# Performance work log

Hardware: AMD Instinct MI355X
Metric: run time of the kernel (lower is better)

## Reference

```python
import jax, jax.numpy as jnp
import numpy as np

B, T, D = 8, 1024, 1024
F = 4 * D  # RWKV channel-mixing hidden size
EPS = 1e-3  # keras LayerNormalization default epsilon


def layer_norm(x, g, b):
    mu = jnp.mean(x, axis=-1, keepdims=True)
    var = jnp.var(x, axis=-1, keepdims=True)
    return (x - mu) * jax.lax.rsqrt(var + EPS) * g + b


def setup_inputs() -> dict:
    key = jax.random.key(0)
    ks = jax.random.split(key, 16)
    s = 0.02
    f32 = jnp.float32
    return {
        "x": jax.random.normal(ks[0], (B, T, D), f32),
        "att_x": jnp.zeros((B, D), f32),
        "att_a": jnp.zeros((B, D), f32),
        "att_b": jnp.zeros((B, D), f32),
        "att_p": jnp.zeros((B, D), f32),
        "ffn_x": jnp.zeros((B, D), f32),
        "ln1_g": jnp.ones((D,), f32),
        "ln1_b": jnp.zeros((D,), f32),
        "ln2_g": jnp.ones((D,), f32),
        "ln2_b": jnp.zeros((D,), f32),
        "tm_mix_k": jax.random.uniform(ks[1], (D,), f32),
        "tm_mix_v": jax.random.uniform(ks[2], (D,), f32),
        "tm_mix_r": jax.random.uniform(ks[3], (D,), f32),
        "tm_decay": jax.random.normal(ks[4], (D,), f32) * 0.1,
        "tm_first": jax.random.normal(ks[5], (D,), f32) * 0.1,
        "Wk": jax.random.normal(ks[6], (D, D), f32) * s,
        "Wv": jax.random.normal(ks[7], (D, D), f32) * s,
        "Wr": jax.random.normal(ks[8], (D, D), f32) * s,
        "Wo": jax.random.normal(ks[9], (D, D), f32) * s,
        "cm_mix_k": jax.random.uniform(ks[10], (D,), f32),
        "cm_mix_r": jax.random.uniform(ks[11], (D,), f32),
        "Ck": jax.random.normal(ks[12], (D, F), f32) * s,
        "Cr": jax.random.normal(ks[13], (D, D), f32) * s,
        "Cv": jax.random.normal(ks[14], (F, D), f32) * s,
    }


def _wkv_scan(k, v, aa, bb, pp, decay, first):
    # k, v: [B, T, D]; states: [B, D]. Numerically-stable RWKV-4 WKV recurrence.
    w = -jnp.exp(decay)  # per-channel decay, always negative

    def step(carry, kv):
        aa, bb, pp = carry
        k_t, v_t = kv
        ww = first + k_t
        p = jnp.maximum(pp, ww)
        e1 = jnp.exp(pp - p)
        e2 = jnp.exp(ww - p)
        wkv = (e1 * aa + e2 * v_t) / (e1 * bb + e2)
        ww2 = pp + w
        p2 = jnp.maximum(ww2, k_t)
        e1b = jnp.exp(ww2 - p2)
        e2b = jnp.exp(k_t - p2)
        return (e1b * aa + e2b * v_t, e1b * bb + e2b, p2), wkv

    kT = jnp.swapaxes(k, 0, 1)  # [T, B, D]
    vT = jnp.swapaxes(v, 0, 1)
    (aa, bb, pp), wkv = jax.lax.scan(step, (aa, bb, pp), (kT, vT))
    return jnp.swapaxes(wkv, 0, 1), aa, bb, pp


def reference(x, att_x, att_a, att_b, att_p, ffn_x,
              ln1_g, ln1_b, ln2_g, ln2_b,
              tm_mix_k, tm_mix_v, tm_mix_r, tm_decay, tm_first,
              Wk, Wv, Wr, Wo, cm_mix_k, cm_mix_r, Ck, Cr, Cv):
    # ---- time mixing (RWKV attention) on ln1(x) ----
    xn = layer_norm(x, ln1_g, ln1_b)  # [B, T, D]
    x_prev = jnp.concatenate([att_x[:, None, :], xn[:, :-1, :]], axis=1)  # token shift
    k = (xn * tm_mix_k + x_prev * (1.0 - tm_mix_k)) @ Wk
    v = (xn * tm_mix_v + x_prev * (1.0 - tm_mix_v)) @ Wv
    r = jax.nn.sigmoid((xn * tm_mix_r + x_prev * (1.0 - tm_mix_r)) @ Wr)
    wkv, aa, bb, pp = _wkv_scan(k, v, att_a, att_b, att_p, tm_decay, tm_first)
    x1 = x + (r * wkv) @ Wo  # residual

    # ---- channel mixing (FFN) on ln2(x1) ----
    xn2 = layer_norm(x1, ln2_g, ln2_b)
    xp = jnp.concatenate([ffn_x[:, None, :], xn2[:, :-1, :]], axis=1)
    kc = jnp.square(jax.nn.relu((xn2 * cm_mix_k + xp * (1.0 - cm_mix_k)) @ Ck))
    rc = jax.nn.sigmoid((xn2 * cm_mix_r + xp * (1.0 - cm_mix_r)) @ Cr)
    out = x1 + rc * (kc @ Cv)

    return (out, xn[:, -1, :], aa, bb, pp, xn2[:, -1, :])
```

## Files before the change

kernel.cpp:

```cpp
#include <hip/hip_runtime.h>

#define TT 1024
#define DD 1024
#define BB 8
#define FF 4096
#define MM (BB * TT)
#define CHL 32
#define NCH (TT / CHL)
#define NCHAN (BB * DD)

typedef unsigned short u16;
typedef unsigned int u32;

typedef __attribute__((ext_vector_type(8))) short short8;
typedef __attribute__((ext_vector_type(4))) float floatx4;

__device__ __forceinline__ u16 f2bf(float f) {
  u32 u = __float_as_uint(f);
  u32 r = (u + 0x7fffu + ((u >> 16) & 1u)) >> 16;
  return (u16)r;
}
__device__ __forceinline__ float bf2f(u16 h) { return __uint_as_float(((u32)h) << 16); }
__device__ __forceinline__ float sigmoidf_(float v) { return 1.0f / (1.0f + __expf(-v)); }

__global__ void transpose_bf16(const float* __restrict__ in, u16* __restrict__ out, int K, int N) {
  __shared__ float tile[32][33];
  int tx = threadIdx.x, ty = threadIdx.y;
  int n0 = blockIdx.x * 32, k0 = blockIdx.y * 32;
#pragma unroll
  for (int j = 0; j < 32; j += 8)
    tile[ty + j][tx] = in[(size_t)(k0 + ty + j) * N + (n0 + tx)];
  __syncthreads();
#pragma unroll
  for (int j = 0; j < 32; j += 8)
    out[(size_t)(n0 + ty + j) * K + (k0 + tx)] = f2bf(tile[tx][ty + j]);
}

__global__ void ln1mix_kernel(const float* __restrict__ x, const float* __restrict__ attx,
                              const float* __restrict__ g, const float* __restrict__ be,
                              const float* __restrict__ mk, const float* __restrict__ mv,
                              const float* __restrict__ mr,
                              u16* __restrict__ xk, u16* __restrict__ xv, u16* __restrict__ xr,
                              float* __restrict__ xn_last) {
  int row = blockIdx.x, tid = threadIdx.x;
  int b = row >> 10, t = row & (TT - 1);
  float4 xc = ((const float4*)(x + (size_t)row * DD))[tid];
  float4 xp = (t == 0) ? ((const float4*)(attx + (size_t)b * DD))[tid]
                       : ((const float4*)(x + (size_t)(row - 1) * DD))[tid];
  float sc = xc.x + xc.y + xc.z + xc.w;
  float qc = xc.x * xc.x + xc.y * xc.y + xc.z * xc.z + xc.w * xc.w;
  float sp = xp.x + xp.y + xp.z + xp.w;
  float qp = xp.x * xp.x + xp.y * xp.y + xp.z * xp.z + xp.w * xp.w;
#pragma unroll
  for (int o = 32; o > 0; o >>= 1) {
    sc += __shfl_xor(sc, o); qc += __shfl_xor(qc, o);
    sp += __shfl_xor(sp, o); qp += __shfl_xor(qp, o);
  }
  __shared__ float red[4][4];
  int lane = tid & 63, wid = tid >> 6;
  if (lane == 0) { red[wid][0] = sc; red[wid][1] = qc; red[wid][2] = sp; red[wid][3] = qp; }
  __syncthreads();
  sc = red[0][0] + red[1][0] + red[2][0] + red[3][0];
  qc = red[0][1] + red[1][1] + red[2][1] + red[3][1];
  sp = red[0][2] + red[1][2] + red[2][2] + red[3][2];
  qp = red[0][3] + red[1][3] + red[2][3] + red[3][3];
  const float inv = 1.0f / (float)DD;
  float muc = sc * inv, varc = qc * inv - muc * muc;
  float rc = rsqrtf(varc + 1e-3f);
  float mup = sp * inv, varp = qp * inv - mup * mup;
  float rp = rsqrtf(varp + 1e-3f);
  float4 gg = ((const float4*)g)[tid];
  float4 bb = ((const float4*)be)[tid];
  float4 k4 = ((const float4*)mk)[tid];
  float4 v4 = ((const float4*)mv)[tid];
  float4 r4 = ((const float4*)mr)[tid];
  float xcv[4] = {xc.x, xc.y, xc.z, xc.w};
  float xpv[4] = {xp.x, xp.y, xp.z, xp.w};
  float gv[4] = {gg.x, gg.y, gg.z, gg.w};
  float bv[4] = {bb.x, bb.y, bb.z, bb.w};
  float kv[4] = {k4.x, k4.y, k4.z, k4.w};
  float vv[4] = {v4.x, v4.y, v4.z, v4.w};
  float rv[4] = {r4.x, r4.y, r4.z, r4.w};
  u16 ok[4], ov[4], orr[4];
  float nc[4];
#pragma unroll
  for (int i = 0; i < 4; i++) {
    nc[i] = (xcv[i] - muc) * rc * gv[i] + bv[i];
    float np = (t == 0) ? xpv[i] : ((xpv[i] - mup) * rp * gv[i] + bv[i]);
    ok[i] = f2bf(nc[i] * kv[i] + np * (1.0f - kv[i]));
    ov[i] = f2bf(nc[i] * vv[i] + np * (1.0f - vv[i]));
    orr[i] = f2bf(nc[i] * rv[i] + np * (1.0f - rv[i]));
  }
  size_t o4 = (size_t)row * (DD / 4) + tid;
  ((ushort4*)xk)[o4] = make_ushort4(ok[0], ok[1], ok[2], ok[3]);
  ((ushort4*)xv)[o4] = make_ushort4(ov[0], ov[1], ov[2], ov[3]);
  ((ushort4*)xr)[o4] = make_ushort4(orr[0], orr[1], orr[2], orr[3]);
  if (t == TT - 1)
    ((float4*)xn_last)[(size_t)b * (DD / 4) + tid] = make_float4(nc[0], nc[1], nc[2], nc[3]);
}

__global__ void ln2mix_kernel(const float* __restrict__ x1, const float* __restrict__ ffnx,
                              const float* __restrict__ g, const float* __restrict__ be,
                              const float* __restrict__ cmk, const float* __restrict__ cmr,
                              u16* __restrict__ xk2, u16* __restrict__ xr2,
                              float* __restrict__ xn2_last) {
  int row = blockIdx.x, tid = threadIdx.x;
  int b = row >> 10, t = row & (TT - 1);
  float4 xc = ((const float4*)(x1 + (size_t)row * DD))[tid];
  float4 xp = (t == 0) ? ((const float4*)(ffnx + (size_t)b * DD))[tid]
                       : ((const float4*)(x1 + (size_t)(row - 1) * DD))[tid];
  float sc = xc.x + xc.y + xc.z + xc.w;
  float qc = xc.x * xc.x + xc.y * xc.y + xc.z * xc.z + xc.w * xc.w;
  float sp = xp.x + xp.y + xp.z + xp.w;
  float qp = xp.x * xp.x + xp.y * xp.y + xp.z * xp.z + xp.w * xp.w;
#pragma unroll
  for (int o = 32; o > 0; o >>= 1) {
    sc += __shfl_xor(sc, o); qc += __shfl_xor(qc, o);
    sp += __shfl_xor(sp, o); qp += __shfl_xor(qp, o);
  }
  __shared__ float red[4][4];
  int lane = tid & 63, wid = tid >> 6;
  if (lane == 0) { red[wid][0] = sc; red[wid][1] = qc; red[wid][2] = sp; red[wid][3] = qp; }
  __syncthreads();
  sc = red[0][0] + red[1][0] + red[2][0] + red[3][0];
  qc = red[0][1] + red[1][1] + red[2][1] + red[3][1];
  sp = red[0][2] + red[1][2] + red[2][2] + red[3][2];
  qp = red[0][3] + red[1][3] + red[2][3] + red[3][3];
  const float inv = 1.0f / (float)DD;
  float muc = sc * inv, varc = qc * inv - muc * muc;
  float rc = rsqrtf(varc + 1e-3f);
  float mup = sp * inv, varp = qp * inv - mup * mup;
  float rp = rsqrtf(varp + 1e-3f);
  float4 gg = ((const float4*)g)[tid];
  float4 bb = ((const float4*)be)[tid];
  float4 k4 = ((const float4*)cmk)[tid];
  float4 r4 = ((const float4*)cmr)[tid];
  float xcv[4] = {xc.x, xc.y, xc.z, xc.w};
  float xpv[4] = {xp.x, xp.y, xp.z, xp.w};
  float gv[4] = {gg.x, gg.y, gg.z, gg.w};
  float bv[4] = {bb.x, bb.y, bb.z, bb.w};
  float kv[4] = {k4.x, k4.y, k4.z, k4.w};
  float rv[4] = {r4.x, r4.y, r4.z, r4.w};
  u16 ok[4], orr[4];
  float nc[4];
#pragma unroll
  for (int i = 0; i < 4; i++) {
    nc[i] = (xcv[i] - muc) * rc * gv[i] + bv[i];
    float np = (t == 0) ? xpv[i] : ((xpv[i] - mup) * rp * gv[i] + bv[i]);
    ok[i] = f2bf(nc[i] * kv[i] + np * (1.0f - kv[i]));
    orr[i] = f2bf(nc[i] * rv[i] + np * (1.0f - rv[i]));
  }
  size_t o4 = (size_t)row * (DD / 4) + tid;
  ((ushort4*)xk2)[o4] = make_ushort4(ok[0], ok[1], ok[2], ok[3]);
  ((ushort4*)xr2)[o4] = make_ushort4(orr[0], orr[1], orr[2], orr[3]);
  if (t == TT - 1)
    ((float4*)xn2_last)[(size_t)b * (DD / 4) + tid] = make_float4(nc[0], nc[1], nc[2], nc[3]);
}


__global__ void wkv_chunk_sum(const float* __restrict__ K, const float* __restrict__ V,
                              const float* __restrict__ decay,
                              float* __restrict__ sa, float* __restrict__ sb,
                              float* __restrict__ ps) {
  int f = blockIdx.x * 256 + threadIdx.x;
  int d = f & (DD - 1);
  int bc = f >> 10;
  int b = bc & (BB - 1);
  int chunk = bc >> 3;
  float w = -__expf(decay[d]);
  const float* kp = K + ((size_t)(b * TT + chunk * CHL)) * DD + d;
  const float* vp = V + ((size_t)(b * TT + chunk * CHL)) * DD + d;
  float aa = 0.0f, bb = 0.0f, pp = -1e30f;
#pragma unroll
  for (int j = 0; j < CHL; j++) {
    float kt = kp[(size_t)j * DD];
    float vt = vp[(size_t)j * DD];
    float ww2 = pp + w;
    float p2 = fmaxf(ww2, kt);
    float e1 = __expf(ww2 - p2);
    float e2 = __expf(kt - p2);
    aa = e1 * aa + e2 * vt;
    bb = e1 * bb + e2;
    pp = p2;
  }
  int ch = b * DD + d;
  size_t s = (size_t)chunk * NCHAN + ch;
  sa[s] = aa; sb[s] = bb; ps[s] = pp;
}

__global__ void wkv_chunk_scan(const float* __restrict__ sa, const float* __restrict__ sb,
                               const float* __restrict__ ps, const float* __restrict__ decay,
                               const float* __restrict__ aa0, const float* __restrict__ bb0,
                               const float* __restrict__ pp0,
                               float* __restrict__ pa, float* __restrict__ pb,
                               float* __restrict__ ppx,
                               float* __restrict__ aa_out, float* __restrict__ bb_out,
                               float* __restrict__ pp_out) {
  int ch = blockIdx.x * 256 + threadIdx.x;
  int d = ch & (DD - 1);
  float w = -__expf(decay[d]);
  float wL = (float)CHL * w;
  float aa = aa0[ch], bb = bb0[ch], pp = pp0[ch];
  float lsa[NCH], lsb[NCH], lps[NCH];
#pragma unroll
  for (int j = 0; j < NCH; j++) {
    size_t s = (size_t)j * NCHAN + ch;
    lsa[j] = sa[s]; lsb[j] = sb[s]; lps[j] = ps[s];
  }
#pragma unroll
  for (int j = 0; j < NCH; j++) {
    size_t s = (size_t)j * NCHAN + ch;
    pa[s] = aa; pb[s] = bb; ppx[s] = pp;
    float pw = pp + wL;
    float pn = fmaxf(pw, lps[j]);
    float e1 = __expf(pw - pn);
    float e2 = __expf(lps[j] - pn);
    aa = e1 * aa + e2 * lsa[j];
    bb = e1 * bb + e2 * lsb[j];
    pp = pn;
  }
  aa_out[ch] = aa; bb_out[ch] = bb; pp_out[ch] = pp;
}

__global__ void wkv_chunk_out(const float* __restrict__ K, const float* __restrict__ V,
                              const u16* __restrict__ sigr, const float* __restrict__ decay,
                              const float* __restrict__ first,
                              const float* __restrict__ pa, const float* __restrict__ pb,
                              const float* __restrict__ ppx, u16* __restrict__ rm) {
  int f = blockIdx.x * 256 + threadIdx.x;
  int d = f & (DD - 1);
  int bc = f >> 10;
  int b = bc & (BB - 1);
  int chunk = bc >> 3;
  float w = -__expf(decay[d]);
  float u = first[d];
  int ch = b * DD + d;
  size_t s = (size_t)chunk * NCHAN + ch;
  float aa = pa[s], bb = pb[s], pp = ppx[s];
  size_t base = ((size_t)(b * TT + chunk * CHL)) * DD + d;
  const float* kp = K + base;
  const float* vp = V + base;
  const u16* rp = sigr + base;
  u16* op = rm + base;
#pragma unroll
  for (int j = 0; j < CHL; j++) {
    float kt = kp[(size_t)j * DD];
    float vt = vp[(size_t)j * DD];
    float ww = u + kt;
    float p = fmaxf(pp, ww);
    float e1 = __expf(pp - p);
    float e2 = __expf(ww - p);
    float wkv = __fdividef(e1 * aa + e2 * vt, e1 * bb + e2);
    op[(size_t)j * DD] = f2bf(bf2f(rp[(size_t)j * DD]) * wkv);
    float ww2 = pp + w;
    float p2 = fmaxf(ww2, kt);
    float e1b = __expf(ww2 - p2);
    float e2b = __expf(kt - p2);
    aa = e1b * aa + e2b * vt;
    bb = e1b * bb + e2b;
    pp = p2;
  }
}


template <int MODE>
__global__ void gemm_bt(const u16* __restrict__ A, const u16* __restrict__ BT,
                        const float* R1, const u16* R2, void* Cout, int M, int N, int K) {
  __shared__ u16 lA[128 * 32];
  __shared__ u16 lB[128 * 32];
  int tid = threadIdx.x;
  int lane = tid & 63;
  int wid = tid >> 6;
  int wy = wid >> 1, wx = wid & 1;
  int m0 = blockIdx.y * 128, n0 = blockIdx.x * 128;
  int rlo = lane & 15;
  int pread = (((lane >> 4) + (rlo >> 1)) & 3) * 8;

  int r1 = tid >> 2, c1 = ((tid & 3) - (r1 >> 1)) & 3;
  int r2 = (256 + tid) >> 2, c2 = (((256 + tid) & 3) - (r2 >> 1)) & 3;
  const u16* gA1 = A + (size_t)(m0 + r1) * K + c1 * 8;
  const u16* gA2 = A + (size_t)(m0 + r2) * K + c2 * 8;
  const u16* gB1 = BT + (size_t)(n0 + r1) * K + c1 * 8;
  const u16* gB2 = BT + (size_t)(n0 + r2) * K + c2 * 8;
  u16* ldsA1 = lA + wid * 512;
  u16* ldsA2 = lA + 2048 + wid * 512;
  u16* ldsB1 = lB + wid * 512;
  u16* ldsB2 = lB + 2048 + wid * 512;

  floatx4 acc[4][4];
#pragma unroll
  for (int mi = 0; mi < 4; mi++)
#pragma unroll
    for (int ni = 0; ni < 4; ni++)
#pragma unroll
      for (int e = 0; e < 4; e++) acc[mi][ni][e] = 0.0f;

  for (int kt = 0; kt < K; kt += 32) {
    __syncthreads();
    __builtin_amdgcn_global_load_lds(gA1 + kt, ldsA1, 16, 0, 0);
    __builtin_amdgcn_global_load_lds(gA2 + kt, ldsA2, 16, 0, 0);
    __builtin_amdgcn_global_load_lds(gB1 + kt, ldsB1, 16, 0, 0);
    __builtin_amdgcn_global_load_lds(gB2 + kt, ldsB2, 16, 0, 0);
    __syncthreads();
    short8 af[4], bfr[4];
#pragma unroll
    for (int mi = 0; mi < 4; mi++)
      af[mi] = *(const short8*)&lA[(wy * 64 + mi * 16 + rlo) * 32 + pread];
#pragma unroll
    for (int ni = 0; ni < 4; ni++)
      bfr[ni] = *(const short8*)&lB[(wx * 64 + ni * 16 + rlo) * 32 + pread];
#pragma unroll
    for (int mi = 0; mi < 4; mi++)
#pragma unroll
      for (int ni = 0; ni < 4; ni++)
        acc[mi][ni] = __builtin_amdgcn_mfma_f32_16x16x32_bf16(af[mi], bfr[ni], acc[mi][ni], 0, 0, 0);
  }

  int rbase = (lane >> 4) * 4;
#pragma unroll
  for (int mi = 0; mi < 4; mi++) {
#pragma unroll
    for (int ni = 0; ni < 4; ni++) {
#pragma unroll
      for (int r = 0; r < 4; r++) {
        int row = m0 + wy * 64 + mi * 16 + rbase + r;
        int col = n0 + wx * 64 + ni * 16 + rlo;
        size_t idx = (size_t)row * N + col;
        float v = acc[mi][ni][r];
        if (MODE == 0) {
          ((float*)Cout)[idx] = v;
        } else if (MODE == 1) {
          ((u16*)Cout)[idx] = f2bf(sigmoidf_(v));
        } else if (MODE == 2) {
          float tpos = fmaxf(v, 0.0f);
          ((u16*)Cout)[idx] = f2bf(tpos * tpos);
        } else if (MODE == 3) {
          ((float*)Cout)[idx] = v + R1[idx];
        } else {
          ((float*)Cout)[idx] = R1[idx] + bf2f(R2[idx]) * v;
        }
      }
    }
  }
}

extern "C" void kernel_launch(void* const* d_in, const int* in_sizes, int n_in,
                              void* d_out, int out_size, void* d_ws, size_t ws_size,
                              hipStream_t stream) {
  const float* x    = (const float*)d_in[0];
  const float* attx = (const float*)d_in[1];
  const float* aa0  = (const float*)d_in[2];
  const float* bb0  = (const float*)d_in[3];
  const float* pp0  = (const float*)d_in[4];
  const float* ffnx = (const float*)d_in[5];
  const float* ln1g = (const float*)d_in[6];
  const float* ln1b = (const float*)d_in[7];
  const float* ln2g = (const float*)d_in[8];
  const float* ln2b = (const float*)d_in[9];
  const float* mk   = (const float*)d_in[10];
  const float* mv   = (const float*)d_in[11];
  const float* mr   = (const float*)d_in[12];
  const float* decay= (const float*)d_in[13];
  const float* first= (const float*)d_in[14];
  const float* Wk   = (const float*)d_in[15];
  const float* Wv   = (const float*)d_in[16];
  const float* Wr   = (const float*)d_in[17];
  const float* Wo   = (const float*)d_in[18];
  const float* cmk  = (const float*)d_in[19];
  const float* cmr  = (const float*)d_in[20];
  const float* Ck   = (const float*)d_in[21];
  const float* Cr   = (const float*)d_in[22];
  const float* Cv   = (const float*)d_in[23];

  float* out      = (float*)d_out;
  float* xn_last  = out + (size_t)BB * TT * DD;
  float* aa_out   = xn_last + BB * DD;
  float* bb_out   = aa_out + BB * DD;
  float* pp_out   = bb_out + BB * DD;
  float* xn2_last = pp_out + BB * DD;
  float* x1 = out;

  char* ws = (char*)d_ws;
  const size_t MB = 1024ull * 1024ull;
  u16* WkT   = (u16*)(ws + 0 * MB);
  u16* WvT   = (u16*)(ws + 2 * MB);
  u16* WrT   = (u16*)(ws + 4 * MB);
  u16* WoT   = (u16*)(ws + 6 * MB);
  u16* CrT   = (u16*)(ws + 8 * MB);
  u16* CkT   = (u16*)(ws + 10 * MB);
  u16* CvT   = (u16*)(ws + 18 * MB);
  u16* xk    = (u16*)(ws + 26 * MB);
  u16* xv    = (u16*)(ws + 42 * MB);
  u16* xr    = (u16*)(ws + 58 * MB);
  float* kbuf= (float*)(ws + 74 * MB);
  float* vbuf= (float*)(ws + 106 * MB);
  u16* sigr  = (u16*)(ws + 138 * MB);
  float* sab = (float*)(ws + 154 * MB);
  float* sbb = (float*)(ws + 155 * MB);
  float* psb = (float*)(ws + 156 * MB);
  float* pab = (float*)(ws + 157 * MB);
  float* pbb = (float*)(ws + 158 * MB);
  float* ppb = (float*)(ws + 159 * MB);
  u16* rmb   = (u16*)(ws + 26 * MB);
  u16* xk2   = (u16*)(ws + 26 * MB);
  u16* xr2   = (u16*)(ws + 42 * MB);
  u16* sigr2 = (u16*)(ws + 58 * MB);
  u16* kc    = (u16*)(ws + 74 * MB);

  dim3 tb32(32, 8);
  transpose_bf16<<<dim3(32, 32), tb32, 0, stream>>>(Wk, WkT, 1024, 1024);
  transpose_bf16<<<dim3(32, 32), tb32, 0, stream>>>(Wv, WvT, 1024, 1024);
  transpose_bf16<<<dim3(32, 32), tb32, 0, stream>>>(Wr, WrT, 1024, 1024);
  transpose_bf16<<<dim3(32, 32), tb32, 0, stream>>>(Wo, WoT, 1024, 1024);
  transpose_bf16<<<dim3(32, 32), tb32, 0, stream>>>(Cr, CrT, 1024, 1024);
  transpose_bf16<<<dim3(128, 32), tb32, 0, stream>>>(Ck, CkT, 1024, 4096);
  transpose_bf16<<<dim3(32, 128), tb32, 0, stream>>>(Cv, CvT, 4096, 1024);

  ln1mix_kernel<<<MM, 256, 0, stream>>>(x, attx, ln1g, ln1b, mk, mv, mr, xk, xv, xr, xn_last);

  gemm_bt<0><<<dim3(8, 64), 256, 0, stream>>>(xk, WkT, nullptr, nullptr, kbuf, MM, 1024, 1024);
  gemm_bt<0><<<dim3(8, 64), 256, 0, stream>>>(xv, WvT, nullptr, nullptr, vbuf, MM, 1024, 1024);
  gemm_bt<1><<<dim3(8, 64), 256, 0, stream>>>(xr, WrT, nullptr, nullptr, sigr, MM, 1024, 1024);

  wkv_chunk_sum<<<NCHAN * NCH / 256, 256, 0, stream>>>(kbuf, vbuf, decay, sab, sbb, psb);
  wkv_chunk_scan<<<NCHAN / 256, 256, 0, stream>>>(sab, sbb, psb, decay, aa0, bb0, pp0,
                                                  pab, pbb, ppb, aa_out, bb_out, pp_out);
  wkv_chunk_out<<<NCHAN * NCH / 256, 256, 0, stream>>>(kbuf, vbuf, sigr, decay, first,
                                                       pab, pbb, ppb, rmb);

  gemm_bt<3><<<dim3(8, 64), 256, 0, stream>>>(rmb, WoT, x, nullptr, x1, MM, 1024, 1024);

  ln2mix_kernel<<<MM, 256, 0, stream>>>(x1, ffnx, ln2g, ln2b, cmk, cmr, xk2, xr2, xn2_last);

  gemm_bt<2><<<dim3(32, 64), 256, 0, stream>>>(xk2, CkT, nullptr, nullptr, kc, MM, 4096, 1024);
  gemm_bt<1><<<dim3(8, 64), 256, 0, stream>>>(xr2, CrT, nullptr, nullptr, sigr2, MM, 1024, 1024);
  gemm_bt<4><<<dim3(8, 64), 256, 0, stream>>>(kc, CvT, x1, sigr2, out, MM, 1024, 4096);
}
```

Measured before the change: 576.3 us.

## Deepen GEMM K-tile to 64, swizzle block order, batch k/v/r GEMMs and transposes

The GEMM now stages a 64-wide K slice per iteration with an 8-way XOR-style LDS swizzle, which halves the number of barrier pairs per K loop. A grouped remapping of block indices is added so that neighbouring blocks share tiles in L2, and launch bounds request three blocks per CU. The three time-mix projection GEMMs are merged into one launch over blockIdx.z, relying on xk/xv/xr and WkT/WvT/WrT sitting contiguously in the workspace. Five of the weight transposes are also merged into one launch. LDS use doubles per block, and the tile remap assumes grid dimensions that fit its hardcoded factor of 8.

```diff
diff --git a/kernel.cpp b/kernel.cpp
--- a/kernel.cpp
+++ b/kernel.cpp
@@ -22,6 +22,24 @@
 }
 __device__ __forceinline__ float bf2f(u16 h) { return __uint_as_float(((u32)h) << 16); }
 __device__ __forceinline__ float sigmoidf_(float v) { return 1.0f / (1.0f + __expf(-v)); }
+
+__global__ void transpose5_bf16(const float* __restrict__ w0, const float* __restrict__ w1,
+                                const float* __restrict__ w2, const float* __restrict__ w3,
+                                const float* __restrict__ w4, u16* __restrict__ outbase) {
+  __shared__ float tile[32][33];
+  const float* srcs[5] = {w0, w1, w2, w3, w4};
+  const float* in = srcs[blockIdx.z];
+  u16* out = outbase + (size_t)blockIdx.z * 1024 * 1024;
+  int tx = threadIdx.x, ty = threadIdx.y;
+  int n0 = blockIdx.x * 32, k0 = blockIdx.y * 32;
+#pragma unroll
+  for (int j = 0; j < 32; j += 8)
+    tile[ty + j][tx] = in[(size_t)(k0 + ty + j) * 1024 + (n0 + tx)];
+  __syncthreads();
+#pragma unroll
+  for (int j = 0; j < 32; j += 8)
+    out[(size_t)(n0 + ty + j) * 1024 + (k0 + tx)] = f2bf(tile[tx][ty + j]);
+}
 
 __global__ void transpose_bf16(const float* __restrict__ in, u16* __restrict__ out, int K, int N) {
   __shared__ float tile[32][33];
@@ -157,7 +175,6 @@
     ((float4*)xn2_last)[(size_t)b * (DD / 4) + tid] = make_float4(nc[0], nc[1], nc[2], nc[3]);
 }
 
-
 __global__ void wkv_chunk_sum(const float* __restrict__ K, const float* __restrict__ V,
                               const float* __restrict__ decay,
                               float* __restrict__ sa, float* __restrict__ sb,
@@ -264,28 +281,44 @@
 
 
 template <int MODE>
-__global__ void gemm_bt(const u16* __restrict__ A, const u16* __restrict__ BT,
-                        const float* R1, const u16* R2, void* Cout, int M, int N, int K) {
-  __shared__ u16 lA[128 * 32];
-  __shared__ u16 lB[128 * 32];
+__launch_bounds__(256, 3)
+__global__ void gemm_bt(const u16* __restrict__ A0, const u16* __restrict__ BT0,
+                        const float* R1, const u16* R2,
+                        void* C0, void* C1, void* C2, int M, int N, int K) {
+  __shared__ u16 lA[128 * 64];
+  __shared__ u16 lB[128 * 64];
   int tid = threadIdx.x;
   int lane = tid & 63;
   int wid = tid >> 6;
   int wy = wid >> 1, wx = wid & 1;
-  int m0 = blockIdx.y * 128, n0 = blockIdx.x * 128;
+
+  const u16* A = A0;
+  const u16* BT = BT0;
+  void* Cout = C0;
+  if (MODE == 5) {
+    int z = blockIdx.z;
+    A = A0 + (size_t)z * M * K;
+    BT = BT0 + (size_t)z * N * K;
+    Cout = (z == 0) ? C0 : (z == 1) ? C1 : C2;
+  }
+
+  int bx = blockIdx.x, by = blockIdx.y;
+  {
+    int flat = by * gridDim.x + bx;
+    int j = flat >> 3;
+    by = (flat & 7) * 8 + (j & 7);
+    bx = j >> 3;
+  }
+  int m0 = by * 128, n0 = bx * 128;
+
   int rlo = lane & 15;
-  int pread = (((lane >> 4) + (rlo >> 1)) & 3) * 8;
-
-  int r1 = tid >> 2, c1 = ((tid & 3) - (r1 >> 1)) & 3;
-  int r2 = (256 + tid) >> 2, c2 = (((256 + tid) & 3) - (r2 >> 1)) & 3;
-  const u16* gA1 = A + (size_t)(m0 + r1) * K + c1 * 8;
-  const u16* gA2 = A + (size_t)(m0 + r2) * K + c2 * 8;
-  const u16* gB1 = BT + (size_t)(n0 + r1) * K + c1 * 8;
-  const u16* gB2 = BT + (size_t)(n0 + r2) * K + c2 * 8;
-  u16* ldsA1 = lA + wid * 512;
-  u16* ldsA2 = lA + 2048 + wid * 512;
-  u16* ldsB1 = lB + wid * 512;
-  u16* ldsB2 = lB + 2048 + wid * 512;
+  int rr = tid >> 3;
+  int cc = ((tid & 7) - rr) & 7;
+  const u16* gA = A + (size_t)(m0 + rr) * K + cc * 8;
+  const u16* gB = BT + (size_t)(n0 + rr) * K + cc * 8;
+  u16* ldsA = lA + wid * 512;
+  u16* ldsB = lB + wid * 512;
+  size_t qstep = (size_t)32 * K;
 
   floatx4 acc[4][4];
 #pragma unroll
@@ -295,25 +328,37 @@
 #pragma unroll
       for (int e = 0; e < 4; e++) acc[mi][ni][e] = 0.0f;
 
-  for (int kt = 0; kt < K; kt += 32) {
+  for (int kt = 0; kt < K; kt += 64) {
     __syncthreads();
-    __builtin_amdgcn_global_load_lds(gA1 + kt, ldsA1, 16, 0, 0);
-    __builtin_amdgcn_global_load_lds(gA2 + kt, ldsA2, 16, 0, 0);
-    __builtin_amdgcn_global_load_lds(gB1 + kt, ldsB1, 16, 0, 0);
-    __builtin_amdgcn_global_load_lds(gB2 + kt, ldsB2, 16, 0, 0);
+#pragma unroll
+    for (int q = 0; q < 4; q++) {
+      __builtin_amdgcn_global_load_lds(gA + q * qstep + kt, ldsA + q * 2048, 16, 0, 0);
+      __builtin_amdgcn_global_load_lds(gB + q * qstep + kt, ldsB + q * 2048, 16, 0, 0);
+    }
     __syncthreads();
-    short8 af[4], bfr[4];
-#pragma unroll
-    for (int mi = 0; mi < 4; mi++)
-      af[mi] = *(const short8*)&lA[(wy * 64 + mi * 16 + rlo) * 32 + pread];
-#pragma unroll
-    for (int ni = 0; ni < 4; ni++)
-      bfr[ni] = *(const short8*)&lB[(wx * 64 + ni * 16 + rlo) * 32 + pread];
-#pragma unroll
-    for (int mi = 0; mi < 4; mi++)
-#pragma unroll
-      for (int ni = 0; ni < 4; ni++)
-        acc[mi][ni] = __builtin_amdgcn_mfma_f32_16x16x32_bf16(af[mi], bfr[ni], acc[mi][ni], 0, 0, 0);
+    short8 af[2][4], bfr[2][4];
+#pragma unroll
+    for (int s = 0; s < 2; s++) {
+      int cbase = s * 4 + (lane >> 4);
+#pragma unroll
+      for (int mi = 0; mi < 4; mi++) {
+        int row = wy * 64 + mi * 16 + rlo;
+        af[s][mi] = *(const short8*)&lA[row * 64 + (((cbase + row) & 7) << 3)];
+      }
+#pragma unroll
+      for (int ni = 0; ni < 4; ni++) {
+        int row = wx * 64 + ni * 16 + rlo;
+        bfr[s][ni] = *(const short8*)&lB[row * 64 + (((cbase + row) & 7) << 3)];
+      }
+    }
+#pragma unroll
+    for (int s = 0; s < 2; s++)
+#pragma unroll
+      for (int mi = 0; mi < 4; mi++)
+#pragma unroll
+        for (int ni = 0; ni < 4; ni++)
+          acc[mi][ni] =
+              __builtin_amdgcn_mfma_f32_16x16x32_bf16(af[s][mi], bfr[s][ni], acc[mi][ni], 0, 0, 0);
   }
 
   int rbase = (lane >> 4) * 4;
@@ -336,8 +381,13 @@
           ((u16*)Cout)[idx] = f2bf(tpos * tpos);
         } else if (MODE == 3) {
           ((float*)Cout)[idx] = v + R1[idx];
+        } else if (MODE == 4) {
+          ((float*)Cout)[idx] = R1[idx] + bf2f(R2[idx]) * v;
         } else {
-          ((float*)Cout)[idx] = R1[idx] + bf2f(R2[idx]) * v;
+          if (blockIdx.z == 2)
+            ((u16*)Cout)[idx] = f2bf(sigmoidf_(v));
+          else
+            ((float*)Cout)[idx] = v;
         }
       }
     }
@@ -382,9 +432,8 @@
 
   char* ws = (char*)d_ws;
   const size_t MB = 1024ull * 1024ull;
-  u16* WkT   = (u16*)(ws + 0 * MB);
-  u16* WvT   = (u16*)(ws + 2 * MB);
-  u16* WrT   = (u16*)(ws + 4 * MB);
+  u16* WT5   = (u16*)(ws + 0 * MB);
+  u16* WkT   = WT5;
   u16* WoT   = (u16*)(ws + 6 * MB);
   u16* CrT   = (u16*)(ws + 8 * MB);
   u16* CkT   = (u16*)(ws + 10 * MB);
@@ -408,19 +457,14 @@
   u16* kc    = (u16*)(ws + 74 * MB);
 
   dim3 tb32(32, 8);
-  transpose_bf16<<<dim3(32, 32), tb32, 0, stream>>>(Wk, WkT, 1024, 1024);
-  transpose_bf16<<<dim3(32, 32), tb32, 0, stream>>>(Wv, WvT, 1024, 1024);
-  transpose_bf16<<<dim3(32, 32), tb32, 0, stream>>>(Wr, WrT, 1024, 1024);
-  transpose_bf16<<<dim3(32, 32), tb32, 0, stream>>>(Wo, WoT, 1024, 1024);
-  transpose_bf16<<<dim3(32, 32), tb32, 0, stream>>>(Cr, CrT, 1024, 1024);
+  transpose5_bf16<<<dim3(32, 32, 5), tb32, 0, stream>>>(Wk, Wv, Wr, Wo, Cr, WT5);
   transpose_bf16<<<dim3(128, 32), tb32, 0, stream>>>(Ck, CkT, 1024, 4096);
   transpose_bf16<<<dim3(32, 128), tb32, 0, stream>>>(Cv, CvT, 4096, 1024);
 
   ln1mix_kernel<<<MM, 256, 0, stream>>>(x, attx, ln1g, ln1b, mk, mv, mr, xk, xv, xr, xn_last);
 
-  gemm_bt<0><<<dim3(8, 64), 256, 0, stream>>>(xk, WkT, nullptr, nullptr, kbuf, MM, 1024, 1024);
-  gemm_bt<0><<<dim3(8, 64), 256, 0, stream>>>(xv, WvT, nullptr, nullptr, vbuf, MM, 1024, 1024);
-  gemm_bt<1><<<dim3(8, 64), 256, 0, stream>>>(xr, WrT, nullptr, nullptr, sigr, MM, 1024, 1024);
+  gemm_bt<5><<<dim3(8, 64, 3), 256, 0, stream>>>(xk, WkT, nullptr, nullptr,
+                                                 kbuf, vbuf, sigr, MM, 1024, 1024);
 
   wkv_chunk_sum<<<NCHAN * NCH / 256, 256, 0, stream>>>(kbuf, vbuf, decay, sab, sbb, psb);
   wkv_chunk_scan<<<NCHAN / 256, 256, 0, stream>>>(sab, sbb, psb, decay, aa0, bb0, pp0,
@@ -428,11 +472,15 @@
   wkv_chunk_out<<<NCHAN * NCH / 256, 256, 0, stream>>>(kbuf, vbuf, sigr, decay, first,
                                                        pab, pbb, ppb, rmb);
 
-  gemm_bt<3><<<dim3(8, 64), 256, 0, stream>>>(rmb, WoT, x, nullptr, x1, MM, 1024, 1024);
+  gemm_bt<3><<<dim3(8, 64), 256, 0, stream>>>(rmb, WoT, x, nullptr, x1, nullptr, nullptr,
+                                              MM, 1024, 1024);
 
   ln2mix_kernel<<<MM, 256, 0, stream>>>(x1, ffnx, ln2g, ln2b, cmk, cmr, xk2, xr2, xn2_last);
 
-  gemm_bt<2><<<dim3(32, 64), 256, 0, stream>>>(xk2, CkT, nullptr, nullptr, kc, MM, 4096, 1024);
-  gemm_bt<1><<<dim3(8, 64), 256, 0, stream>>>(xr2, CrT, nullptr, nullptr, sigr2, MM, 1024, 1024);
-  gemm_bt<4><<<dim3(8, 64), 256, 0, stream>>>(kc, CvT, x1, sigr2, out, MM, 1024, 4096);
-}
+  gemm_bt<2><<<dim3(32, 64), 256, 0, stream>>>(xk2, CkT, nullptr, nullptr, kc, nullptr, nullptr,
+                                               MM, 4096, 1024);
+  gemm_bt<1><<<dim3(8, 64), 256, 0, stream>>>(xr2, CrT, nullptr, nullptr, sigr2, nullptr, nullptr,
+                                              MM, 1024, 1024);
+  gemm_bt<4><<<dim3(8, 64), 256, 0, stream>>>(kc, CvT, x1, sigr2, out, nullptr, nullptr,
+                                              MM, 1024, 4096);
+}
```

Measured after the change: 511.8 us. 11.2% less time.
